# Optimization experiments

Hardware: AMD Instinct MI355X
Metric: run time of the kernel (lower is better)

Reference implementation:

```python
import jax, jax.numpy as jnp
import numpy as np

BATCH = 262144

def _f64_bits_msb_first(val):
    # IEEE754 double bit pattern, MSB first (equivalent to struct.pack('>d', val))
    u = int(np.frombuffer(np.float64(val).tobytes(), dtype=np.uint64)[0])
    return [float((u >> (63 - i)) & 1) for i in range(64)]

def setup_inputs() -> dict:
    key = jax.random.key(0)
    # Table T[j] = bits of 2^(j/64), shape [64 entries, 64 bits]
    table = np.array([_f64_bits_msb_first(2.0 ** (j / 64.0)) for j in range(64)],
                     dtype=np.float32)
    idx_bits = jax.random.randint(key, (BATCH, 6), 0, 2).astype(jnp.int32)
    return {"table_bits": jnp.asarray(table), "idx_bits": idx_bits}

def reference(table_bits, idx_bits):
    """Fused MUX-tree table lookup.

    Each MUXGate(sel, B, A) = sel ? B : A on binary pulses. Level k selects on
    idx_bits[..., k] (MSB first) between the lower and upper half of the
    surviving table entries, exactly reproducing the 6-level tree of 64-bit MUXes.
    """
    batch_shape = idx_bits.shape[:-1]
    # [B, 64 entries, 64 bits]
    x = jnp.broadcast_to(table_bits, batch_shape + table_bits.shape)
    for k in range(6):  # b5 (weight 32) down to b0 (weight 1)
        n = x.shape[-2] // 2
        sel = (idx_bits[..., k] > 0)[..., None, None]
        x = jnp.where(sel, x[..., n:, :], x[..., :n, :])
    return x[..., 0, :]  # [B, 64] bit pulses of 2^(idx/64)
```

## Files before the change

kernel.cpp:

```cpp
#include <hip/hip_runtime.h>


#define ROWS 256

__global__ __launch_bounds__(256) void
spike_lut_kernel(const float* __restrict__ table,
                 const int* __restrict__ idx_bits,
                 float4* __restrict__ out4,
                 int batch) {
    __shared__ float4 s_table[64 * 16];
    __shared__ int    s_raw[ROWS * 6];
    __shared__ int    s_idx[ROWS];

    const int  tid = threadIdx.x;
    const long b0  = (long)blockIdx.x * ROWS;
    const bool full = (b0 + ROWS) <= batch;

    const float4* t4 = (const float4*)table;
    #pragma unroll
    for (int r = 0; r < 4; ++r)
        s_table[r * 256 + tid] = t4[r * 256 + tid];

    const int* src = idx_bits + b0 * 6;
    if (full) {
        #pragma unroll
        for (int r = 0; r < 6; ++r)
            s_raw[r * 256 + tid] = src[r * 256 + tid];
    } else {
        const long lim = ((long)batch - b0) * 6;
        #pragma unroll
        for (int r = 0; r < 6; ++r) {
            const int g = r * 256 + tid;
            s_raw[g] = (g < lim) ? src[g] : 0;
        }
    }
    __syncthreads();

    {
        const int* p = &s_raw[tid * 6];
        int idx = 0;
        #pragma unroll
        for (int k = 0; k < 6; ++k)
            idx = (idx << 1) | (p[k] > 0 ? 1 : 0);
        s_idx[tid] = idx;
    }
    __syncthreads();

    if (full) {
        #pragma unroll
        for (int it = 0; it < 16; ++it) {
            const int g  = it * 256 + tid;
            const int bl = g >> 4;
            const int q  = g & 15;
            out4[(b0 + bl) * 16 + q] = s_table[s_idx[bl] * 16 + q];
        }
    } else {
        #pragma unroll
        for (int it = 0; it < 16; ++it) {
            const int g  = it * 256 + tid;
            const int bl = g >> 4;
            const int q  = g & 15;
            if (b0 + bl < batch)
                out4[(b0 + bl) * 16 + q] = s_table[s_idx[bl] * 16 + q];
        }
    }
}

extern "C" void kernel_launch(void* const* d_in, const int* in_sizes, int n_in,
                              void* d_out, int out_size, void* d_ws, size_t ws_size,
                              hipStream_t stream) {
    const float* table    = (const float*)d_in[0];
    const int*   idx_bits = (const int*)d_in[1];
    float4*      out4     = (float4*)d_out;

    const int batch  = in_sizes[1] / 6;
    const int blocks = (batch + ROWS - 1) / ROWS;

    spike_lut_kernel<<<blocks, 256, 0, stream>>>(table, idx_bits, out4, batch);
}
```

Measured before the change: 80.19 us.

## Compress table to 64-bit ballot masks and use nontemporal output stores

Each block now packs the 64x64 float table into 64 bitmasks with wave ballots instead of copying 16 KB of float4 into shared memory. Index bits are read directly per thread from global memory instead of being staged through shared memory. Output floats are rebuilt from mask bits and written with nontemporal stores to avoid polluting the cache. This relies on the table holding only 0/1 values, so any fractional entry would be rounded by the >0.5 threshold, and the direct per-row index loads are strided and less coalesced.

```diff
diff --git a/kernel.cpp b/kernel.cpp
--- a/kernel.cpp
+++ b/kernel.cpp
@@ -3,45 +3,39 @@
 
 #define ROWS 256
 
+typedef float nfloat4 __attribute__((ext_vector_type(4)));
+
 __global__ __launch_bounds__(256) void
 spike_lut_kernel(const float* __restrict__ table,
                  const int* __restrict__ idx_bits,
-                 float4* __restrict__ out4,
+                 nfloat4* __restrict__ out4,
                  int batch) {
-    __shared__ float4 s_table[64 * 16];
-    __shared__ int    s_raw[ROWS * 6];
-    __shared__ int    s_idx[ROWS];
+    __shared__ unsigned long long s_mask[64];
+    __shared__ int s_idx[ROWS];
 
-    const int  tid = threadIdx.x;
-    const long b0  = (long)blockIdx.x * ROWS;
+    const int  tid  = threadIdx.x;
+    const int  wave = tid >> 6;
+    const int  lane = tid & 63;
+    const long b0   = (long)blockIdx.x * ROWS;
     const bool full = (b0 + ROWS) <= batch;
 
-    const float4* t4 = (const float4*)table;
     #pragma unroll
-    for (int r = 0; r < 4; ++r)
-        s_table[r * 256 + tid] = t4[r * 256 + tid];
-
-    const int* src = idx_bits + b0 * 6;
-    if (full) {
-        #pragma unroll
-        for (int r = 0; r < 6; ++r)
-            s_raw[r * 256 + tid] = src[r * 256 + tid];
-    } else {
-        const long lim = ((long)batch - b0) * 6;
-        #pragma unroll
-        for (int r = 0; r < 6; ++r) {
-            const int g = r * 256 + tid;
-            s_raw[g] = (g < lim) ? src[g] : 0;
-        }
+    for (int i = 0; i < 16; ++i) {
+        const int row = wave * 16 + i;
+        const float f = table[row * 64 + lane];
+        const unsigned long long m = __ballot(f > 0.5f);
+        if (lane == 0) s_mask[row] = m;
     }
-    __syncthreads();
 
     {
-        const int* p = &s_raw[tid * 6];
         int idx = 0;
-        #pragma unroll
-        for (int k = 0; k < 6; ++k)
-            idx = (idx << 1) | (p[k] > 0 ? 1 : 0);
+        const long b = b0 + tid;
+        if (b < (long)batch) {
+            const int* p = idx_bits + b * 6;
+            #pragma unroll
+            for (int k = 0; k < 6; ++k)
+                idx = (idx << 1) | (p[k] > 0 ? 1 : 0);
+        }
         s_idx[tid] = idx;
     }
     __syncthreads();
@@ -52,7 +46,13 @@
             const int g  = it * 256 + tid;
             const int bl = g >> 4;
             const int q  = g & 15;
-            out4[(b0 + bl) * 16 + q] = s_table[s_idx[bl] * 16 + q];
+            const unsigned int r = (unsigned int)(s_mask[s_idx[bl]] >> (q * 4));
+            nfloat4 v;
+            v.x = (r & 1u) ? 1.0f : 0.0f;
+            v.y = (r & 2u) ? 1.0f : 0.0f;
+            v.z = (r & 4u) ? 1.0f : 0.0f;
+            v.w = (r & 8u) ? 1.0f : 0.0f;
+            __builtin_nontemporal_store(v, &out4[(b0 + bl) * 16 + q]);
         }
     } else {
         #pragma unroll
@@ -60,8 +60,15 @@
             const int g  = it * 256 + tid;
             const int bl = g >> 4;
             const int q  = g & 15;
-            if (b0 + bl < batch)
-                out4[(b0 + bl) * 16 + q] = s_table[s_idx[bl] * 16 + q];
+            if (b0 + bl < batch) {
+                const unsigned int r = (unsigned int)(s_mask[s_idx[bl]] >> (q * 4));
+                nfloat4 v;
+                v.x = (r & 1u) ? 1.0f : 0.0f;
+                v.y = (r & 2u) ? 1.0f : 0.0f;
+                v.z = (r & 4u) ? 1.0f : 0.0f;
+                v.w = (r & 8u) ? 1.0f : 0.0f;
+                __builtin_nontemporal_store(v, &out4[(b0 + bl) * 16 + q]);
+            }
         }
     }
 }
@@ -71,7 +78,7 @@
                               hipStream_t stream) {
     const float* table    = (const float*)d_in[0];
     const int*   idx_bits = (const int*)d_in[1];
-    float4*      out4     = (float4*)d_out;
+    nfloat4*     out4     = (nfloat4*)d_out;
 
     const int batch  = in_sizes[1] / 6;
     const int blocks = (batch + ROWS - 1) / ROWS;
```

Measured after the change: 87.51 us. +9.1%, slower.
